# Optimization experiments

Measured on AMD Instinct MI355X. Metric: run time of the kernel, lower is better.

The kernel has to match this reference:

```python
import jax, jax.numpy as jnp
import numpy as np

EMBED_DIM = 1024
HEAD_DIM = 64


def setup_inputs() -> dict:
    key = jax.random.key(0)
    k1, k2, k3, k4 = jax.random.split(key, 4)
    B, T = 4, 4096
    x = jax.random.normal(k1, (B, T, EMBED_DIM), dtype=jnp.float32)
    # nn.Linear(EMBED_DIM, head_dim, bias=False): store as (EMBED_DIM, head_dim)
    s = (1.0 / np.sqrt(EMBED_DIM)).astype(np.float32)
    Wk = jax.random.uniform(k2, (EMBED_DIM, HEAD_DIM), jnp.float32, -s, s)
    Wq = jax.random.uniform(k3, (EMBED_DIM, HEAD_DIM), jnp.float32, -s, s)
    Wv = jax.random.uniform(k4, (EMBED_DIM, HEAD_DIM), jnp.float32, -s, s)
    return {"x": x, "Wq": Wq, "Wk": Wk, "Wv": Wv}


def reference(x, Wq, Wk, Wv):
    B, T, E = x.shape
    q = jnp.einsum('bte,ed->btd', x, Wq)  # (B,T,D)
    k = jnp.einsum('bte,ed->btd', x, Wk)
    v = jnp.einsum('bte,ed->btd', x, Wv)
    # NOTE: original scales by EMBED_DIM**-0.5 (x.size(-1)), not head_dim**-0.5
    scale = jnp.asarray(E, x.dtype) ** -0.5
    scores = jnp.einsum('bqd,bkd->bqk', q, k) * scale  # (B,T,T)
    causal = jnp.tril(jnp.ones((T, T), dtype=bool))
    scores = jnp.where(causal, scores, jnp.asarray(-jnp.inf, scores.dtype))
    attn = jax.nn.softmax(scores, axis=-1)
    # dropout is identity at inference (deterministic baseline)
    out = jnp.einsum('bqk,bkd->bqd', attn, v)  # (B,T,D)
    return out
```

## Files before the change

### kernel.cpp

```cpp
#include <hip/hip_runtime.h>
#include <hip/hip_bf16.h>
#include <stdint.h>

#define BATCH 4
#define SEQ   4096
#define EMB   1024
#define HD    64

typedef __bf16 bf16x8 __attribute__((ext_vector_type(8)));
typedef float  f32x4  __attribute__((ext_vector_type(4)));
typedef unsigned short u16;

union ABFrag { u16 s[8]; bf16x8 v; };

__device__ __forceinline__ u16 f2bf_rne(float f) {
    union { float f; uint32_t u; } cv; cv.f = f;
    uint32_t u = cv.u;
    return (u16)((u + 0x7fffu + ((u >> 16) & 1u)) >> 16);
}
__device__ __forceinline__ float bf2f(u16 h) {
    union { uint32_t u; float f; } cv; cv.u = ((uint32_t)h) << 16;
    return cv.f;
}
__device__ __forceinline__ void gld16(const void* g, void* l) {
    __builtin_amdgcn_global_load_lds(
        (const __attribute__((address_space(1))) void*)g,
        (__attribute__((address_space(3))) void*)l, 16, 0, 0);
}

__global__ __launch_bounds__(256) void wt_kernel(
        const float* __restrict__ Wq, const float* __restrict__ Wk,
        const float* __restrict__ Wv, u16* __restrict__ Wt) {
    int idx = blockIdx.x * 256 + threadIdx.x;
    int i = idx >> 16;
    int r = idx & 65535;
    int n = r >> 10;
    int k = r & 1023;
    const float* W = (i == 0) ? Wq : (i == 1) ? Wk : Wv;
    Wt[idx] = f2bf_rne(W[k * HD + n]);
}

__global__ __launch_bounds__(512) void qkv_kernel(
        const float* __restrict__ x, const u16* __restrict__ Wt,
        u16* __restrict__ Qw, u16* __restrict__ Kw, u16* __restrict__ Vt) {
    __shared__ u16 wl[64 * 1032];

    const int t    = threadIdx.x;
    const int wave = t >> 6;
    const int lane = t & 63;
    const int m16  = lane & 15;
    const int quad = lane >> 4;
    const int wv   = blockIdx.x >> 6;
    const int rb   = blockIdx.x & 63;

    {
        const u16* wsrc = Wt + (wv << 16);
#pragma unroll
        for (int j = 0; j < 16; ++j) {
            const int idx = (wave << 4) + j;
            const int n   = idx >> 1;
            const int hh  = idx & 1;
            gld16(wsrc + (n << 10) + (hh << 9) + (lane << 3),
                  &wl[n * 1032 + (hh << 9)]);
        }
    }
    __syncthreads();

    const int rtA  = (rb << 4) + (wave << 1);
    const int rowA = (rtA << 4) + m16;
    const float* xpA = x + (size_t)rowA * EMB + (quad << 3);
    const float* xpB = xpA + (16 * EMB);

    f32x4 accA[4], accB[4];
#pragma unroll
    for (int tt = 0; tt < 4; ++tt) {
        accA[tt] = (f32x4){0.f, 0.f, 0.f, 0.f};
        accB[tt] = (f32x4){0.f, 0.f, 0.f, 0.f};
    }

    const u16* wbase = &wl[m16 * 1032 + (quad << 3)];

#pragma unroll 2
    for (int kt = 0; kt < 32; ++kt) {
        const float4 a0A = *(const float4*)(xpA + (kt << 5));
        const float4 a1A = *(const float4*)(xpA + (kt << 5) + 4);
        const float4 a0B = *(const float4*)(xpB + (kt << 5));
        const float4 a1B = *(const float4*)(xpB + (kt << 5) + 4);
        ABFrag afA, afB;
        afA.s[0] = f2bf_rne(a0A.x); afA.s[1] = f2bf_rne(a0A.y);
        afA.s[2] = f2bf_rne(a0A.z); afA.s[3] = f2bf_rne(a0A.w);
        afA.s[4] = f2bf_rne(a1A.x); afA.s[5] = f2bf_rne(a1A.y);
        afA.s[6] = f2bf_rne(a1A.z); afA.s[7] = f2bf_rne(a1A.w);
        afB.s[0] = f2bf_rne(a0B.x); afB.s[1] = f2bf_rne(a0B.y);
        afB.s[2] = f2bf_rne(a0B.z); afB.s[3] = f2bf_rne(a0B.w);
        afB.s[4] = f2bf_rne(a1B.x); afB.s[5] = f2bf_rne(a1B.y);
        afB.s[6] = f2bf_rne(a1B.z); afB.s[7] = f2bf_rne(a1B.w);
#pragma unroll
        for (int tt = 0; tt < 4; ++tt) {
            const bf16x8 bf = *(const bf16x8*)(wbase + tt * (16 * 1032) + (kt << 5));
            accA[tt] = __builtin_amdgcn_mfma_f32_16x16x32_bf16(afA.v, bf, accA[tt], 0, 0, 0);
            accB[tt] = __builtin_amdgcn_mfma_f32_16x16x32_bf16(afB.v, bf, accB[tt], 0, 0, 0);
        }
    }

#pragma unroll
    for (int half = 0; half < 2; ++half) {
        const f32x4* acc = half ? accB : accA;
        const int rowbase = ((rtA + half) << 4) + (quad << 2);
        const int bidx = rowbase >> 12;
        const int t0   = rowbase & 4095;
#pragma unroll
        for (int tt = 0; tt < 4; ++tt) {
            const int col = (tt << 4) + m16;
            if (wv == 0) {
#pragma unroll
                for (int reg = 0; reg < 4; ++reg)
                    Qw[(size_t)(rowbase + reg) * HD + col] = f2bf_rne(acc[tt][reg] * 0.03125f);
            } else if (wv == 1) {
#pragma unroll
                for (int reg = 0; reg < 4; ++reg)
                    Kw[(size_t)(rowbase + reg) * HD + col] = f2bf_rne(acc[tt][reg]);
            } else {
                ushort4 vv;
                vv.x = f2bf_rne(acc[tt][0]); vv.y = f2bf_rne(acc[tt][1]);
                vv.z = f2bf_rne(acc[tt][2]); vv.w = f2bf_rne(acc[tt][3]);
                *(ushort4*)(Vt + (size_t)((bidx << 6) + col) * SEQ + t0) = vv;
            }
        }
    }
}

__global__ __launch_bounds__(512) void attn_part_kernel(
        const u16* __restrict__ Qw, const u16* __restrict__ Kw,
        const u16* __restrict__ Vt, u16* __restrict__ Opart,
        float* __restrict__ Mp, float* __restrict__ Lp) {
    __shared__ u16 kv[2][2][4096];
    __shared__ u16 ldsP[8][16 * 72];

    const int pid = blockIdx.x;
    const int r   = pid >> 8;
    const int s   = pid & 255;
    const int b   = s >> 6;
    const int i0  = (s >> 1) & 31;
    const int ch  = s & 1;
    const int i   = r ? (31 - i0) : i0;
    const int c   = (ch << 1) | r;
    const int jmax = (i << 1) + 1;
    const int p_out = (((b << 5) + i) << 2) + c;

    const int wave = threadIdx.x >> 6;
    const int lane = threadIdx.x & 63;
    const int m16  = lane & 15;
    const int quad = lane >> 4;
    const int jend = (i << 1) + (wave >> 2);

    #define ISSUE_KV(buf_, jt_) do {                                           \
        const int r8_ = lane >> 3, c8_ = lane & 7;                             \
        const int kc_ = c8_ ^ r8_;                                             \
        const int row_ = (wave << 3) + r8_;                         \
        gld16(Kw + ((size_t)(b * SEQ + ((jt_) << 6) + row_) << 6) + (kc_ << 3),\
              &kv[buf_][0][wave << 9]);                                        \
        gld16(Vt + (size_t)((b << 6) + row_) * SEQ + ((jt_) << 6) + (kc_ << 3),\
              &kv[buf_][1][wave << 9]);                                        \
    } while (0)

    const int qrow = (i << 7) + (wave << 4) + m16;
    const u16* qbase = Qw + ((size_t)(b * SEQ + qrow) << 6);
    const bf16x8 qf0 = *(const bf16x8*)(qbase + (quad << 3));
    const bf16x8 qf1 = *(const bf16x8*)(qbase + 32 + (quad << 3));

    f32x4 acc[4];
#pragma unroll
    for (int dt = 0; dt < 4; ++dt) acc[dt] = (f32x4){0.f, 0.f, 0.f, 0.f};
    float m_i = -3.0e38f;
    float l_i = 0.f;

    u16* ldsW = &ldsP[wave][0];
    const int xs0 = (quad ^ (m16 & 7)) << 3;
    const int xs1 = ((quad + 4) ^ (m16 & 7)) << 3;

    if (c <= jmax) ISSUE_KV(0, c);

    int buf = 0;
    for (int jt = c; jt <= jmax; jt += 4) {
        __syncthreads();
        if (jt + 4 <= jmax) ISSUE_KV(buf ^ 1, jt + 4);

        if (jt <= jend) {
            f32x4 sv[4];
#pragma unroll
            for (int mt = 0; mt < 4; ++mt) {
                const int base = ((mt << 4) + m16) << 6;
                bf16x8 k0 = *(const bf16x8*)&kv[buf][0][base + xs0];
                bf16x8 k1 = *(const bf16x8*)&kv[buf][0][base + xs1];
                sv[mt] = (f32x4){0.f, 0.f, 0.f, 0.f};
                sv[mt] = __builtin_amdgcn_mfma_f32_16x16x32_bf16(k0, qf0, sv[mt], 0, 0, 0);
                sv[mt] = __builtin_amdgcn_mfma_f32_16x16x32_bf16(k1, qf1, sv[mt], 0, 0, 0);
            }

            if (jt == jend) {
                const int q_in = ((wave & 3) << 4) + m16;
#pragma unroll
                for (int mt = 0; mt < 4; ++mt) {
                    const int k_in = (mt << 4) + (quad << 2);
#pragma unroll
                    for (int reg = 0; reg < 4; ++reg)
                        if (k_in + reg > q_in) sv[mt][reg] = -3.0e38f;
                }
            }

            float tm = fmaxf(fmaxf(sv[0][0], sv[0][1]), fmaxf(sv[0][2], sv[0][3]));
#pragma unroll
            for (int mt = 1; mt < 4; ++mt)
                tm = fmaxf(tm, fmaxf(fmaxf(sv[mt][0], sv[mt][1]), fmaxf(sv[mt][2], sv[mt][3])));
            tm = fmaxf(tm, __shfl_xor(tm, 16));
            tm = fmaxf(tm, __shfl_xor(tm, 32));

            const float mnew  = fmaxf(m_i, tm);
            const float alpha = __expf(m_i - mnew);
            m_i = mnew;

            float psum = 0.f;
#pragma unroll
            for (int mt = 0; mt < 4; ++mt) {
                const float p0 = __expf(sv[mt][0] - mnew);
                const float p1 = __expf(sv[mt][1] - mnew);
                const float p2 = __expf(sv[mt][2] - mnew);
                const float p3 = __expf(sv[mt][3] - mnew);
                psum += (p0 + p1) + (p2 + p3);
                ushort4 pv;
                pv.x = f2bf_rne(p0); pv.y = f2bf_rne(p1);
                pv.z = f2bf_rne(p2); pv.w = f2bf_rne(p3);
                *(ushort4*)(ldsW + m16 * 72 + (mt << 4) + (quad << 2)) = pv;
            }
            l_i = l_i * alpha + psum;
#pragma unroll
            for (int dt = 0; dt < 4; ++dt)
#pragma unroll
                for (int reg = 0; reg < 4; ++reg) acc[dt][reg] *= alpha;

            const bf16x8 p0 = *(const bf16x8*)(ldsW + m16 * 72 + (quad << 3));
            const bf16x8 p1 = *(const bf16x8*)(ldsW + m16 * 72 + 32 + (quad << 3));
#pragma unroll
            for (int dt = 0; dt < 4; ++dt) {
                const int base = ((dt << 4) + m16) << 6;
                bf16x8 v0 = *(const bf16x8*)&kv[buf][1][base + xs0];
                bf16x8 v1 = *(const bf16x8*)&kv[buf][1][base + xs1];
                acc[dt] = __builtin_amdgcn_mfma_f32_16x16x32_bf16(v0, p0, acc[dt], 0, 0, 0);
                acc[dt] = __builtin_amdgcn_mfma_f32_16x16x32_bf16(v1, p1, acc[dt], 0, 0, 0);
            }
        }
        buf ^= 1;
    }
    #undef ISSUE_KV

    float l = l_i;
    l += __shfl_xor(l, 16);
    l += __shfl_xor(l, 32);

    u16* ob = Opart + ((size_t)p_out << 13);
    const int qin = (wave << 4) + m16;
#pragma unroll
    for (int dt = 0; dt < 4; ++dt) {
        ushort4 vv;
        vv.x = f2bf_rne(acc[dt][0]); vv.y = f2bf_rne(acc[dt][1]);
        vv.z = f2bf_rne(acc[dt][2]); vv.w = f2bf_rne(acc[dt][3]);
        *(ushort4*)(ob + qin * 64 + (dt << 4) + (quad << 2)) = vv;
    }
    if (quad == 0) {
        Mp[(p_out << 7) + qin] = m_i;
        Lp[(p_out << 7) + qin] = l;
    }
}

__global__ __launch_bounds__(256) void combine_kernel(
        const u16* __restrict__ Opart, const float* __restrict__ Mp,
        const float* __restrict__ Lp, float* __restrict__ out) {
    __shared__ float sm[4][16];
    __shared__ float sl[4][16];
    const int bi = blockIdx.x >> 3;
    const int rq = blockIdx.x & 7;
    const int pidbase = bi << 2;
    const int t = threadIdx.x;
    if (t < 64) {
        const int cc = t >> 4, rr = t & 15;
        sm[cc][rr] = Mp[((pidbase + cc) << 7) + (rq << 4) + rr];
        sl[cc][rr] = Lp[((pidbase + cc) << 7) + (rq << 4) + rr];
    }
    __syncthreads();

    const int row_l = t >> 4;
    const int c4    = (t & 15) << 2;
    const int row   = (rq << 4) + row_l;

    const float M = fmaxf(fmaxf(sm[0][row_l], sm[1][row_l]),
                          fmaxf(sm[2][row_l], sm[3][row_l]));
    float n0 = 0.f, n1 = 0.f, n2 = 0.f, n3 = 0.f, den = 0.f;
#pragma unroll
    for (int cc = 0; cc < 4; ++cc) {
        const float w = __expf(sm[cc][row_l] - M);
        den += w * sl[cc][row_l];
        const ushort4 op = *(const ushort4*)&Opart[
                ((size_t)(pidbase + cc) << 13) + row * 64 + c4];
        n0 += w * bf2f(op.x); n1 += w * bf2f(op.y);
        n2 += w * bf2f(op.z); n3 += w * bf2f(op.w);
    }
    const float rd = 1.0f / den;
    float4 o; o.x = n0 * rd; o.y = n1 * rd; o.z = n2 * rd; o.w = n3 * rd;
    const int brow = (bi >> 5) * SEQ + ((bi & 31) << 7) + row;
    *(float4*)&out[((size_t)brow << 6) + c4] = o;
}

extern "C" void kernel_launch(void* const* d_in, const int* in_sizes, int n_in,
                              void* d_out, int out_size, void* d_ws, size_t ws_size,
                              hipStream_t stream) {
    const float* x  = (const float*)d_in[0];
    const float* Wq = (const float*)d_in[1];
    const float* Wk = (const float*)d_in[2];
    const float* Wv = (const float*)d_in[3];
    float* out = (float*)d_out;

    char* ws = (char*)d_ws;
    u16* Qw    = (u16*)(ws);
    u16* Kw    = (u16*)(ws + (2u << 20));
    u16* Vt    = (u16*)(ws + (4u << 20));
    u16* Wt    = (u16*)(ws + (6u << 20));
    u16* Opart = (u16*)(ws + (13u << 19));
    float* Mp  = (float*)(ws + (29u << 19));
    float* Lp  = (float*)(ws + (59u << 18));

    wt_kernel<<<768, 256, 0, stream>>>(Wq, Wk, Wv, Wt);
    qkv_kernel<<<192, 512, 0, stream>>>(x, Wt, Qw, Kw, Vt);
    attn_part_kernel<<<512, 512, 0, stream>>>(Qw, Kw, Vt, Opart, Mp, Lp);
    combine_kernel<<<1024, 256, 0, stream>>>(Opart, Mp, Lp, out);
}
```

Before: 153.9 us.

## Fuse weight conversion into QKV and split-K combine into attention via counters

Removes the separate weight-transpose kernel by having each QKV block load fp32 weights, convert them to bf16 and transpose them into LDS itself. Also removes the combine kernel: each attention block bumps an atomic counter after writing its partial, and the last of the four chunk blocks for a query tile performs the softmax-merge and writes the output. This saves two launches and the gaps between them, at the cost of a memset launch, redundant weight conversion in every QKV block, scattered 2-byte LDS stores, and a serial combine tail inside the final block.

```diff
diff --git a/kernel.cpp b/kernel.cpp
--- a/kernel.cpp
+++ b/kernel.cpp
@@ -28,20 +28,9 @@
         (__attribute__((address_space(3))) void*)l, 16, 0, 0);
 }
 
-__global__ __launch_bounds__(256) void wt_kernel(
-        const float* __restrict__ Wq, const float* __restrict__ Wk,
-        const float* __restrict__ Wv, u16* __restrict__ Wt) {
-    int idx = blockIdx.x * 256 + threadIdx.x;
-    int i = idx >> 16;
-    int r = idx & 65535;
-    int n = r >> 10;
-    int k = r & 1023;
-    const float* W = (i == 0) ? Wq : (i == 1) ? Wk : Wv;
-    Wt[idx] = f2bf_rne(W[k * HD + n]);
-}
-
 __global__ __launch_bounds__(512) void qkv_kernel(
-        const float* __restrict__ x, const u16* __restrict__ Wt,
+        const float* __restrict__ x,  const float* __restrict__ Wq,
+        const float* __restrict__ Wk, const float* __restrict__ Wv,
         u16* __restrict__ Qw, u16* __restrict__ Kw, u16* __restrict__ Vt) {
     __shared__ u16 wl[64 * 1032];
 
@@ -54,14 +43,17 @@
     const int rb   = blockIdx.x & 63;
 
     {
-        const u16* wsrc = Wt + (wv << 16);
-#pragma unroll
-        for (int j = 0; j < 16; ++j) {
-            const int idx = (wave << 4) + j;
-            const int n   = idx >> 1;
-            const int hh  = idx & 1;
-            gld16(wsrc + (n << 10) + (hh << 9) + (lane << 3),
-                  &wl[n * 1032 + (hh << 9)]);
+        const float* Wsrc = (wv == 0) ? Wq : (wv == 1) ? Wk : Wv;
+        const int kk0 = t >> 4;
+        const int n0  = (t & 15) << 2;
+#pragma unroll 4
+        for (int it = 0; it < 32; ++it) {
+            const int kk = (it << 5) + kk0;
+            const float4 w4 = *(const float4*)(Wsrc + kk * HD + n0);
+            wl[(n0 + 0) * 1032 + kk] = f2bf_rne(w4.x);
+            wl[(n0 + 1) * 1032 + kk] = f2bf_rne(w4.y);
+            wl[(n0 + 2) * 1032 + kk] = f2bf_rne(w4.z);
+            wl[(n0 + 3) * 1032 + kk] = f2bf_rne(w4.w);
         }
     }
     __syncthreads();
@@ -130,12 +122,14 @@
     }
 }
 
-__global__ __launch_bounds__(512) void attn_part_kernel(
+__global__ __launch_bounds__(512) void attn_kernel(
         const u16* __restrict__ Qw, const u16* __restrict__ Kw,
         const u16* __restrict__ Vt, u16* __restrict__ Opart,
-        float* __restrict__ Mp, float* __restrict__ Lp) {
+        float* __restrict__ Mp, float* __restrict__ Lp,
+        int* __restrict__ counters, float* __restrict__ out) {
     __shared__ u16 kv[2][2][4096];
     __shared__ u16 ldsP[8][16 * 72];
+    __shared__ int lastflag;
 
     const int pid = blockIdx.x;
     const int r   = pid >> 8;
@@ -271,44 +265,53 @@
         Mp[(p_out << 7) + qin] = m_i;
         Lp[(p_out << 7) + qin] = l;
     }
-}
-
-__global__ __launch_bounds__(256) void combine_kernel(
-        const u16* __restrict__ Opart, const float* __restrict__ Mp,
-        const float* __restrict__ Lp, float* __restrict__ out) {
-    __shared__ float sm[4][16];
-    __shared__ float sl[4][16];
-    const int bi = blockIdx.x >> 3;
-    const int rq = blockIdx.x & 7;
-    const int pidbase = bi << 2;
-    const int t = threadIdx.x;
-    if (t < 64) {
-        const int cc = t >> 4, rr = t & 15;
-        sm[cc][rr] = Mp[((pidbase + cc) << 7) + (rq << 4) + rr];
-        sl[cc][rr] = Lp[((pidbase + cc) << 7) + (rq << 4) + rr];
+
+    __threadfence();
+    if (threadIdx.x == 0) {
+        lastflag = (__hip_atomic_fetch_add(&counters[(b << 5) + i], 1,
+                        __ATOMIC_ACQ_REL, __HIP_MEMORY_SCOPE_AGENT) == 3);
     }
     __syncthreads();
-
-    const int row_l = t >> 4;
-    const int c4    = (t & 15) << 2;
-    const int row   = (rq << 4) + row_l;
-
-    const float M = fmaxf(fmaxf(sm[0][row_l], sm[1][row_l]),
-                          fmaxf(sm[2][row_l], sm[3][row_l]));
-    float n0 = 0.f, n1 = 0.f, n2 = 0.f, n3 = 0.f, den = 0.f;
-#pragma unroll
-    for (int cc = 0; cc < 4; ++cc) {
-        const float w = __expf(sm[cc][row_l] - M);
-        den += w * sl[cc][row_l];
-        const ushort4 op = *(const ushort4*)&Opart[
-                ((size_t)(pidbase + cc) << 13) + row * 64 + c4];
-        n0 += w * bf2f(op.x); n1 += w * bf2f(op.y);
-        n2 += w * bf2f(op.z); n3 += w * bf2f(op.w);
-    }
-    const float rd = 1.0f / den;
-    float4 o; o.x = n0 * rd; o.y = n1 * rd; o.z = n2 * rd; o.w = n3 * rd;
-    const int brow = (bi >> 5) * SEQ + ((bi & 31) << 7) + row;
-    *(float4*)&out[((size_t)brow << 6) + c4] = o;
+    if (lastflag) {
+        const int pb  = ((b << 5) + i) << 2;
+        const int row = threadIdx.x & 127;
+        const int g4  = (threadIdx.x >> 7) << 4;
+        float ms[4], lsv[4];
+        float M = -3.0e38f;
+#pragma unroll
+        for (int cc = 0; cc < 4; ++cc) {
+            ms[cc]  = Mp[((pb + cc) << 7) + row];
+            lsv[cc] = Lp[((pb + cc) << 7) + row];
+            M = fmaxf(M, ms[cc]);
+        }
+        float num[16];
+#pragma unroll
+        for (int v = 0; v < 16; ++v) num[v] = 0.f;
+        float den = 0.f;
+#pragma unroll
+        for (int cc = 0; cc < 4; ++cc) {
+            const float w = __expf(ms[cc] - M);
+            den += w * lsv[cc];
+            const u16* op = Opart + ((size_t)(pb + cc) << 13) + row * 64 + g4;
+#pragma unroll
+            for (int v = 0; v < 4; ++v) {
+                const ushort4 o4 = *(const ushort4*)(op + (v << 2));
+                num[v * 4 + 0] += w * bf2f(o4.x);
+                num[v * 4 + 1] += w * bf2f(o4.y);
+                num[v * 4 + 2] += w * bf2f(o4.z);
+                num[v * 4 + 3] += w * bf2f(o4.w);
+            }
+        }
+        const float rd = 1.0f / den;
+        float* obp = out + ((size_t)(b * SEQ + (i << 7) + row) << 6) + g4;
+#pragma unroll
+        for (int v = 0; v < 4; ++v) {
+            float4 o;
+            o.x = num[v * 4 + 0] * rd; o.y = num[v * 4 + 1] * rd;
+            o.z = num[v * 4 + 2] * rd; o.w = num[v * 4 + 3] * rd;
+            *(float4*)(obp + (v << 2)) = o;
+        }
+    }
 }
 
 extern "C" void kernel_launch(void* const* d_in, const int* in_sizes, int n_in,
@@ -321,16 +324,15 @@
     float* out = (float*)d_out;
 
     char* ws = (char*)d_ws;
-    u16* Qw    = (u16*)(ws);
-    u16* Kw    = (u16*)(ws + (2u << 20));
-    u16* Vt    = (u16*)(ws + (4u << 20));
-    u16* Wt    = (u16*)(ws + (6u << 20));
-    u16* Opart = (u16*)(ws + (13u << 19));
-    float* Mp  = (float*)(ws + (29u << 19));
-    float* Lp  = (float*)(ws + (59u << 18));
-
-    wt_kernel<<<768, 256, 0, stream>>>(Wq, Wk, Wv, Wt);
-    qkv_kernel<<<192, 512, 0, stream>>>(x, Wt, Qw, Kw, Vt);
-    attn_part_kernel<<<512, 512, 0, stream>>>(Qw, Kw, Vt, Opart, Mp, Lp);
-    combine_kernel<<<1024, 256, 0, stream>>>(Opart, Mp, Lp, out);
-}
+    u16* Qw     = (u16*)(ws);
+    u16* Kw     = (u16*)(ws + (2u << 20));
+    u16* Vt     = (u16*)(ws + (4u << 20));
+    u16* Opart  = (u16*)(ws + (13u << 19));
+    float* Mp   = (float*)(ws + (29u << 19));
+    float* Lp   = (float*)(ws + (59u << 18));
+    int* counters = (int*)(ws + (15u << 20));
+
+    hipMemsetAsync(counters, 0, 128 * sizeof(int), stream);
+    qkv_kernel<<<192, 512, 0, stream>>>(x, Wq, Wk, Wv, Qw, Kw, Vt);
+    attn_kernel<<<512, 512, 0, stream>>>(Qw, Kw, Vt, Opart, Mp, Lp, counters, out);
+}
```

Measured after the change: 302.7 us. +96.7%, slower.
